# Kernel tuning notes

Hardware: AMD Instinct MI355X
Metric: run time of the kernel (lower is better)

Reference implementation:

```python
import jax, jax.numpy as jnp
import numpy as np
import math

B, S, E = 2, 2048, 1024
H, D = 16, 64
LAMBDA_INIT = 0.8
GN_EPS = 1e-5


def setup_inputs() -> dict:
    key = jax.random.key(0)
    ks = jax.random.split(key, 12)
    s = 0.02
    inputs = jax.random.normal(ks[0], (B, S, E), jnp.float32)
    attention_mask = jnp.ones((B, S), jnp.float32)
    token_indices = jnp.sort(jax.random.randint(ks[1], (B, S), 0, S), axis=-1)
    Wq = jax.random.normal(ks[2], (2 * H * D, E), jnp.float32) * s
    Wk = jax.random.normal(ks[3], (2 * H * D, E), jnp.float32) * s
    Wv = jax.random.normal(ks[4], (H * D, E), jnp.float32) * s
    Wo = jax.random.normal(ks[5], (E, H * D), jnp.float32) * s
    lam_q1 = jax.random.normal(ks[6], (D,), jnp.float32) * 0.1
    lam_q2 = jax.random.normal(ks[7], (D,), jnp.float32) * 0.1
    lam_k1 = jax.random.normal(ks[8], (D,), jnp.float32) * 0.1
    lam_k2 = jax.random.normal(ks[9], (D,), jnp.float32) * 0.1
    gn_w = jnp.ones((H * D,), jnp.float32)
    gn_b = jnp.zeros((H * D,), jnp.float32)
    return dict(inputs=inputs, attention_mask=attention_mask, token_indices=token_indices,
                Wq=Wq, Wk=Wk, Wv=Wv, Wo=Wo,
                lam_q1=lam_q1, lam_q2=lam_q2, lam_k1=lam_k1, lam_k2=lam_k2,
                gn_w=gn_w, gn_b=gn_b)


def reference(inputs, attention_mask, token_indices, Wq, Wk, Wv, Wo,
              lam_q1, lam_q2, lam_k1, lam_k2, gn_w, gn_b):
    b, s, e = inputs.shape
    # projections: q,k have doubled head dim (differential), v is standard
    q = (inputs @ Wq.T).reshape(b, s, H, 2 * D).transpose(0, 2, 1, 3)  # [B,H,S,2D]
    k = (inputs @ Wk.T).reshape(b, s, H, 2 * D).transpose(0, 2, 1, 3)
    v = (inputs @ Wv.T).reshape(b, s, H, D).transpose(0, 2, 1, 3)      # [B,H,S,D]
    Q1, Q2 = q[..., :D], q[..., D:]
    K1, K2 = k[..., :D], k[..., D:]
    scale = 1.0 / math.sqrt(D)
    s1 = jnp.einsum('bhqd,bhkd->bhqk', Q1, K1) * scale
    s2 = jnp.einsum('bhqd,bhkd->bhqk', Q2, K2) * scale
    # ALiBi bias: slopes[h] * (pos_q - pos_k), subtracted
    slopes = 2.0 ** (-8.0 * jnp.arange(1, H + 1, dtype=jnp.float32) / H)
    pos = token_indices.astype(jnp.float32)                            # [B,S]
    pos_diff = pos[:, :, None] - pos[:, None, :]                       # [B,S,S]
    bias = slopes[None, :, None, None] * pos_diff[:, None, :, :]       # [B,H,S,S]
    # causal + padding masks
    causal = jnp.triu(jnp.full((s, s), -1e9, jnp.float32), 1)[None, None]
    pad = (1.0 - attention_mask)[:, None, None, :] * -1e9
    s1 = s1 - bias + causal + pad
    s2 = s2 - bias + causal + pad
    w1 = jax.nn.softmax(s1, axis=-1)
    w2 = jax.nn.softmax(s2, axis=-1)
    lam = jnp.exp(jnp.dot(lam_q1, lam_k1)) - jnp.exp(jnp.dot(lam_q2, lam_k2)) + LAMBDA_INIT
    w = w1 - lam * w2
    out = jnp.einsum('bhqk,bhkd->bhqd', w, v)                          # [B,H,S,D]
    # GroupNorm(num_groups=H, num_channels=H*D) over channels-first layout [B,C,S]
    x = out.transpose(0, 2, 1, 3).reshape(b, s, H * D).transpose(0, 2, 1)  # [B,C,S]
    xg = x.reshape(b, H, D * s)
    mean = xg.mean(axis=-1, keepdims=True)
    var = xg.var(axis=-1, keepdims=True)
    xn = ((xg - mean) / jnp.sqrt(var + GN_EPS)).reshape(b, H * D, s)
    xn = xn * gn_w[None, :, None] + gn_b[None, :, None]
    xn = xn * (1.0 - LAMBDA_INIT)
    attn = xn.transpose(0, 2, 1)                                       # [B,S,H*D]
    return attn @ Wo.T
```

## Files before the change

kernel.cpp:

```cpp
#include <hip/hip_runtime.h>
#include <hip/hip_bf16.h>

typedef __hip_bfloat16 bf16;
typedef float f32x4 __attribute__((ext_vector_type(4)));
typedef float fvec4 __attribute__((ext_vector_type(4)));
typedef short s16x8 __attribute__((ext_vector_type(8)));

#define NB_B 2
#define NB_S 2048
#define NB_E 1024
#define NB_H 16
#define NB_D 64

typedef const __attribute__((address_space(1))) void* GPTR;
typedef __attribute__((address_space(3))) void* LPTR;

__device__ __forceinline__ void gld16(const void* g, void* l) {
  __builtin_amdgcn_global_load_lds((GPTR)g, (LPTR)l, 16, 0, 0);
}

__device__ __forceinline__ s16x8 ld8(const bf16* p) { return *(const s16x8*)p; }

__device__ __forceinline__ f32x4 MFMA(s16x8 a, s16x8 b, f32x4 c) {
  return __builtin_amdgcn_mfma_f32_16x16x32_bf16(a, b, c, 0, 0, 0);
}

struct __align__(8) bf16x4 { bf16 a, b, c, d; };

__global__ void prep_kernel(const float* __restrict__ inputs,
                            const float* __restrict__ wq, const float* __restrict__ wk,
                            const float* __restrict__ wv, const float* __restrict__ wo,
                            const float* __restrict__ lq1, const float* __restrict__ lq2,
                            const float* __restrict__ lk1, const float* __restrict__ lk2,
                            bf16* __restrict__ xbf,
                            bf16* __restrict__ oq, bf16* __restrict__ ok,
                            bf16* __restrict__ ov, bf16* __restrict__ oo,
                            float* __restrict__ lamo) {
  const int blk = blockIdx.x;
  if (blk < 4096) {
    int i = blk * 256 + threadIdx.x;
    fvec4 v = ((const fvec4*)inputs)[i];
    bf16x4 o = { bf16(v.x), bf16(v.y), bf16(v.z), bf16(v.w) };
    ((bf16x4*)xbf)[i] = o;
  } else if (blk < 10240) {
    int i = (blk - 4096) * 256 + threadIdx.x;
    const float* src; bf16* dst; int off;
    if (i < 524288)       { src = wq; dst = oq; off = i; }
    else if (i < 1048576) { src = wk; dst = ok; off = i - 524288; }
    else if (i < 1310720) { src = wv; dst = ov; off = i - 1048576; }
    else                  { src = wo; dst = oo; off = i - 1310720; }
    fvec4 v = ((const fvec4*)src)[off];
    bf16x4 o = { bf16(v.x), bf16(v.y), bf16(v.z), bf16(v.w) };
    ((bf16x4*)dst)[off] = o;
  } else {
    int l = threadIdx.x;
    if (l < 64) {
      float d1 = lq1[l] * lk1[l];
      float d2 = lq2[l] * lk2[l];
#pragma unroll
      for (int o = 32; o; o >>= 1) { d1 += __shfl_xor(d1, o); d2 += __shfl_xor(d2, o); }
      if (l == 0) lamo[0] = expf(d1) - expf(d2) + 0.8f;
    }
  }
}

__global__ void combo_kernel(const int* __restrict__ tok, const float* __restrict__ amask,
                             float* __restrict__ combo) {
  int i = blockIdx.x * 256 + threadIdx.x;
  int hh = i >> 12, bs = i & 4095;
  float slopeL = exp2f(-0.5f * (float)(hh + 1)) * 1.44269504088896340736f;
  combo[i] = slopeL * (float)tok[bs] + (amask[bs] - 1.f) * 1.44269504e9f;
}

template <int EPI>
__global__ __launch_bounds__(256) void gemm_bt(const bf16* __restrict__ A,
                                               const bf16* __restrict__ Bw,
                                               bf16* __restrict__ Ob,
                                               bf16* __restrict__ Ob2,
                                               bf16* __restrict__ Ob3,
                                               float* __restrict__ Of,
                                               int Kd, float oscale) {
  __shared__ bf16 As[2][128 * 32];
  __shared__ bf16 Bs[2][128 * 32];
  const int tid = threadIdx.x;
  const int lane = tid & 63;
  const int fr = lane & 15, fq = lane >> 4;
  const int wave = tid >> 6;
  const int wr = (wave >> 1) * 64, wc = (wave & 1) * 64;
  const size_t m0 = (size_t)blockIdx.x * 128, n0 = (size_t)blockIdx.y * 128;

  f32x4 acc[4][4];
#pragma unroll
  for (int i = 0; i < 4; i++)
#pragma unroll
    for (int j = 0; j < 4; j++) acc[i][j] = f32x4{0.f, 0.f, 0.f, 0.f};

  const int ca = tid, cb = tid + 256;
  const bf16* ga0 = A + (m0 + (ca >> 2)) * Kd + (ca & 3) * 8;
  const bf16* ga1 = A + (m0 + (cb >> 2)) * Kd + (cb & 3) * 8;
  const bf16* gb0 = Bw + (n0 + (ca >> 2)) * Kd + (ca & 3) * 8;
  const bf16* gb1 = Bw + (n0 + (cb >> 2)) * Kd + (cb & 3) * 8;

  gld16(ga0, &As[0][ca * 8]);
  gld16(ga1, &As[0][cb * 8]);
  gld16(gb0, &Bs[0][ca * 8]);
  gld16(gb1, &Bs[0][cb * 8]);
  __syncthreads();

  const int NKT = Kd >> 5;
  for (int kti = 0; kti < NKT; ++kti) {
    const int cur = kti & 1;
    if (kti + 1 < NKT) {
      const int kt = (kti + 1) << 5;
      gld16(ga0 + kt, &As[cur ^ 1][ca * 8]);
      gld16(ga1 + kt, &As[cur ^ 1][cb * 8]);
      gld16(gb0 + kt, &Bs[cur ^ 1][ca * 8]);
      gld16(gb1 + kt, &Bs[cur ^ 1][cb * 8]);
    }
    s16x8 af[4], bfv[4];
#pragma unroll
    for (int mi = 0; mi < 4; mi++) af[mi] = ld8(&As[cur][(wr + mi * 16 + fr) * 32 + fq * 8]);
#pragma unroll
    for (int ni = 0; ni < 4; ni++) bfv[ni] = ld8(&Bs[cur][(wc + ni * 16 + fr) * 32 + fq * 8]);
#pragma unroll
    for (int mi = 0; mi < 4; mi++)
#pragma unroll
      for (int ni = 0; ni < 4; ni++)
        acc[mi][ni] = MFMA(af[mi], bfv[ni], acc[mi][ni]);
    __syncthreads();
  }

  bf16* dst = Ob;
  size_t nsub = 0;
  float osc = oscale;
  bool isV = false;
  if constexpr (EPI == 0) {
    if (n0 >= 4096)      { dst = Ob3; nsub = 4096; osc = 1.0f; isV = true; }
    else if (n0 >= 2048) { dst = Ob2; nsub = 2048; osc = 1.0f; }
  }

  if constexpr (EPI == 0) {
    if (isV) {
#pragma unroll
      for (int mi = 0; mi < 4; mi++)
#pragma unroll
        for (int ni = 0; ni < 4; ni++) {
          size_t m = m0 + wr + mi * 16 + fq * 4;
          size_t n = n0 + wc + ni * 16 + fr;
          size_t nn = n - 4096;
          size_t b = m >> 11, s = m & 2047, h = nn >> 6, d = nn & 63;
          bf16x4 o = { bf16(acc[mi][ni][0]), bf16(acc[mi][ni][1]),
                       bf16(acc[mi][ni][2]), bf16(acc[mi][ni][3]) };
          *(bf16x4*)&dst[((b * NB_H + h) * NB_D + d) * NB_S + s] = o;
        }
    } else {
#pragma unroll
      for (int mi = 0; mi < 4; mi++)
#pragma unroll
        for (int ni = 0; ni < 4; ni++)
#pragma unroll
          for (int i = 0; i < 4; i++) {
            size_t m = m0 + wr + mi * 16 + fq * 4 + i;
            size_t n = n0 + wc + ni * 16 + fr;
            float v = acc[mi][ni][i] * osc;
            size_t nn = n - nsub;
            size_t b = m >> 11, s = m & 2047, h = nn >> 7, dd = nn & 127;
            dst[((b * NB_H + h) * NB_S + s) * 128 + dd] = bf16(v);
          }
    }
  } else {
#pragma unroll
    for (int mi = 0; mi < 4; mi++)
#pragma unroll
      for (int ni = 0; ni < 4; ni++)
#pragma unroll
        for (int i = 0; i < 4; i++) {
          size_t m = m0 + wr + mi * 16 + fq * 4 + i;
          size_t n = n0 + wc + ni * 16 + fr;
          Of[m * 1024 + n] = acc[mi][ni][i] * oscale;
        }
  }
}

__global__ __launch_bounds__(512, 2) void attn_kernel(
    const bf16* __restrict__ Q, const bf16* __restrict__ Kk, const bf16* __restrict__ Vt,
    const float* __restrict__ combo,
    const float* __restrict__ lamp, bf16* __restrict__ Xb, float* __restrict__ gnp) {
  __shared__ bf16 Ks[2][2][4096];
  __shared__ bf16 Vs[2][4096];
  __shared__ bf16 Ps[8][1024];
  __shared__ float gs[8][2];

  const int tid = threadIdx.x, lane = tid & 63, wave = tid >> 6;
  const int fr = lane & 15, fq = lane >> 4;
  const int id = blockIdx.x;
  const int w = id >> 3;
  const int bh = (id & 7) * 4 + (w & 3);
  const int qj = 15 - (w >> 2);
  const int b = bh >> 4, h = bh & 15;

  const float lam = lamp[0];
  const float* comboH = combo + ((size_t)h * NB_B + b) * NB_S;

  const bf16* Kbase = Kk + (size_t)bh * NB_S * 128;
  const bf16* Vbase = Vt + (size_t)bh * NB_D * NB_S;

  const s16x8 onesv = { 0x3F80, 0x3F80, 0x3F80, 0x3F80, 0x3F80, 0x3F80, 0x3F80, 0x3F80 };

  int adr[4][2], pw[4], pr[2];
#pragma unroll
  for (int nt = 0; nt < 4; nt++) {
    const int r = nt * 16 + fr;
#pragma unroll
    for (int kk = 0; kk < 2; kk++) adr[nt][kk] = r * 64 + (((kk * 4 + fq) ^ (r & 7)) << 3);
    pw[nt] = fr * 64 + (((nt * 4 + fq) ^ ((fr & 7) << 1)) << 2);
  }
  pr[0] = fr * 64 + (((fq * 2) ^ ((fr & 7) << 1)) << 2);
  pr[1] = fr * 64 + (((8 + fq * 2) ^ ((fr & 7) << 1)) << 2);

  const bf16* gK[2]; int lK[2];
#pragma unroll
  for (int i = 0; i < 2; i++) {
    int c = tid + i * 512, set = c >> 9, cc = c & 511;
    int row = cc >> 3, col8 = cc & 7, sc = col8 ^ (row & 7);
    gK[i] = Kbase + (size_t)row * 128 + set * 64 + sc * 8;
    lK[i] = set * 4096 + cc * 8;
  }
  const bf16* gV; int lV;
  {
    int c = tid;
    int row = c >> 3, col8 = c & 7, sc = col8 ^ (row & 7);
    gV = Vbase + (size_t)row * NB_S + sc * 8;
    lV = c * 8;
  }

  const int q0 = qj * 128;
  const int qw = q0 + wave * 16;
  const int ntiles = 2 * qj + 2;

  const bf16* qrow = Q + ((size_t)bh * NB_S + qw + fr) * 128;
  s16x8 q1[2], q2[2];
  q1[0] = ld8(qrow + fq * 8);       q1[1] = ld8(qrow + 32 + fq * 8);
  q2[0] = ld8(qrow + 64 + fq * 8);  q2[1] = ld8(qrow + 96 + fq * 8);

  const int qg = qw + fr;

  float m1 = -1e30f, m2 = -1e30f;
  f32x4 acc1[4], acc2[4];
  f32x4 accL1 = f32x4{0.f,0.f,0.f,0.f}, accL2 = f32x4{0.f,0.f,0.f,0.f};
#pragma unroll
  for (int nt = 0; nt < 4; nt++) { acc1[nt] = f32x4{0.f,0.f,0.f,0.f}; acc2[nt] = f32x4{0.f,0.f,0.f,0.f}; }

#pragma unroll
  for (int i = 0; i < 2; i++) gld16(gK[i], &Ks[0][0][0] + lK[i]);
  gld16(gV, &Vs[0][0] + lV);
  fvec4 cmb[4];
#pragma unroll
  for (int nt = 0; nt < 4; nt++) cmb[nt] = *(const fvec4*)(comboH + nt * 16 + fq * 4);
  __syncthreads();

  for (int t = 0; t < ntiles; ++t) {
    const int cur = t & 1;
    const int kv0 = t * 64;
    if (t + 1 < ntiles) {
#pragma unroll
      for (int i = 0; i < 2; i++)
        gld16(gK[i] + (size_t)(kv0 + 64) * 128, &Ks[cur ^ 1][0][0] + lK[i]);
      gld16(gV + (size_t)(kv0 + 64), &Vs[cur ^ 1][0] + lV);
    }

    const bool active = (kv0 <= qw + 15);
    if (active) {
      const bf16* kb0 = &Ks[cur][0][0];
      const bf16* kb1 = &Ks[cur][1][0];

      f32x4 c1[4], c2[4];
      __builtin_amdgcn_s_setprio(1);
#pragma unroll
      for (int nt = 0; nt < 4; nt++) {
        c1[nt] = MFMA(ld8(kb0 + adr[nt][0]), q1[0], cmb[nt]);
        c2[nt] = MFMA(ld8(kb1 + adr[nt][0]), q2[0], cmb[nt]);
      }
      {
        const float* cp = comboH + (t + 1 < ntiles ? kv0 + 64 : kv0);
#pragma unroll
        for (int nt = 0; nt < 4; nt++) cmb[nt] = *(const fvec4*)(cp + nt * 16 + fq * 4);
      }
#pragma unroll
      for (int nt = 0; nt < 4; nt++) {
        c1[nt] = MFMA(ld8(kb0 + adr[nt][1]), q1[1], c1[nt]);
        c2[nt] = MFMA(ld8(kb1 + adr[nt][1]), q2[1], c2[nt]);
      }
      __builtin_amdgcn_s_setprio(0);

      if (kv0 + 63 > qw) {
#pragma unroll
        for (int nt = 0; nt < 4; nt++)
#pragma unroll
          for (int i = 0; i < 4; i++)
            if (kv0 + nt * 16 + fq * 4 + i > qg) { c1[nt][i] = -1e30f; c2[nt][i] = -1e30f; }
      }

      s16x8 vf[4][2];
#pragma unroll
      for (int nt = 0; nt < 4; nt++)
#pragma unroll
        for (int kk = 0; kk < 2; kk++)
          vf[nt][kk] = ld8(&Vs[cur][adr[nt][kk]]);

      {
        float pm = fmaxf(fmaxf(fmaxf(c1[0][0], c1[0][1]), fmaxf(c1[0][2], c1[0][3])),
                         fmaxf(fmaxf(c1[1][0], c1[1][1]), fmaxf(c1[1][2], c1[1][3])));
        pm = fmaxf(pm, fmaxf(fmaxf(fmaxf(c1[2][0], c1[2][1]), fmaxf(c1[2][2], c1[2][3])),
                             fmaxf(fmaxf(c1[3][0], c1[3][1]), fmaxf(c1[3][2], c1[3][3]))));
        pm = fmaxf(pm, __shfl_xor(pm, 16));
        pm = fmaxf(pm, __shfl_xor(pm, 32));
        if (__any(pm > m1 + 8.f)) {
          const float nm = fmaxf(m1, pm);
          const float cor = exp2f(m1 - nm);
          m1 = nm;
#pragma unroll
          for (int i = 0; i < 4; i++) {
            const float ci = __shfl(cor, fq * 4 + i);
            accL1[i] *= ci;
#pragma unroll
            for (int nt = 0; nt < 4; nt++) acc1[nt][i] *= ci;
          }
        }
#pragma unroll
        for (int nt = 0; nt < 4; nt++) {
          bf16x4 pk = { bf16(exp2f(c1[nt][0] - m1)), bf16(exp2f(c1[nt][1] - m1)),
                        bf16(exp2f(c1[nt][2] - m1)), bf16(exp2f(c1[nt][3] - m1)) };
          *(bf16x4*)&Ps[wave][pw[nt]] = pk;
        }
        __builtin_amdgcn_s_setprio(1);
#pragma unroll
        for (int kk = 0; kk < 2; kk++) {
          const s16x8 pa = ld8(&Ps[wave][pr[kk]]);
          accL1 = MFMA(pa, onesv, accL1);
#pragma unroll
          for (int nt = 0; nt < 4; nt++) acc1[nt] = MFMA(pa, vf[nt][kk], acc1[nt]);
        }
        __builtin_amdgcn_s_setprio(0);
      }
      {
        float pm = fmaxf(fmaxf(fmaxf(c2[0][0], c2[0][1]), fmaxf(c2[0][2], c2[0][3])),
                         fmaxf(fmaxf(c2[1][0], c2[1][1]), fmaxf(c2[1][2], c2[1][3])));
        pm = fmaxf(pm, fmaxf(fmaxf(fmaxf(c2[2][0], c2[2][1]), fmaxf(c2[2][2], c2[2][3])),
                             fmaxf(fmaxf(c2[3][0], c2[3][1]), fmaxf(c2[3][2], c2[3][3]))));
        pm = fmaxf(pm, __shfl_xor(pm, 16));
        pm = fmaxf(pm, __shfl_xor(pm, 32));
        if (__any(pm > m2 + 8.f)) {
          const float nm = fmaxf(m2, pm);
          const float cor = exp2f(m2 - nm);
          m2 = nm;
#pragma unroll
          for (int i = 0; i < 4; i++) {
            const float ci = __shfl(cor, fq * 4 + i);
            accL2[i] *= ci;
#pragma unroll
            for (int nt = 0; nt < 4; nt++) acc2[nt][i] *= ci;
          }
        }
#pragma unroll
        for (int nt = 0; nt < 4; nt++) {
          bf16x4 pk = { bf16(exp2f(c2[nt][0] - m2)), bf16(exp2f(c2[nt][1] - m2)),
                        bf16(exp2f(c2[nt][2] - m2)), bf16(exp2f(c2[nt][3] - m2)) };
          *(bf16x4*)&Ps[wave][pw[nt]] = pk;
        }
        __builtin_amdgcn_s_setprio(1);
#pragma unroll
        for (int kk = 0; kk < 2; kk++) {
          const s16x8 pa = ld8(&Ps[wave][pr[kk]]);
          accL2 = MFMA(pa, onesv, accL2);
#pragma unroll
          for (int nt = 0; nt < 4; nt++) acc2[nt] = MFMA(pa, vf[nt][kk], acc2[nt]);
        }
        __builtin_amdgcn_s_setprio(0);
      }
    }

    __syncthreads();
  }

  float r1b[4], r2b[4];
#pragma unroll
  for (int i = 0; i < 4; i++) { r1b[i] = 1.f / accL1[i]; r2b[i] = lam / accL2[i]; }
  float s = 0.f, s2 = 0.f;
#pragma unroll
  for (int nt = 0; nt < 4; nt++)
#pragma unroll
    for (int i = 0; i < 4; i++) {
      const float v = acc1[nt][i] * r1b[i] - acc2[nt][i] * r2b[i];
      Xb[((size_t)bh * NB_S + qw + fq * 4 + i) * NB_D + nt * 16 + fr] = bf16(v);
      s += v; s2 += v * v;
    }
#pragma unroll
  for (int o = 32; o; o >>= 1) { s += __shfl_xor(s, o); s2 += __shfl_xor(s2, o); }
  if (lane == 0) { gs[wave][0] = s; gs[wave][1] = s2; }
  __syncthreads();
  if (tid == 0) {
    float S = 0.f, S2 = 0.f;
#pragma unroll
    for (int i = 0; i < 8; i++) { S += gs[i][0]; S2 += gs[i][1]; }
    atomicAdd(&gnp[bh * 2], S);
    atomicAdd(&gnp[bh * 2 + 1], S2);
  }
}

__global__ __launch_bounds__(256) void gn_apply(const bf16* __restrict__ Xb,
                                                const float* __restrict__ gnp,
                                                const float* __restrict__ gw,
                                                const float* __restrict__ gb,
                                                bf16* __restrict__ Xn) {
  const int blk = blockIdx.x, bh = blk >> 3, seg = blk & 7;
  const int b = bh >> 4, h = bh & 15;
  const float mean = gnp[bh * 2] * (1.f / 131072.f);
  const float var = gnp[bh * 2 + 1] * (1.f / 131072.f) - mean * mean;
  const float rstd = rsqrtf(var + 1e-5f) * 0.2f;
  const int tid = threadIdx.x;
  const int d0 = (tid * 8) & 63;
  const int c = h * 64 + d0;
  fvec4 w0 = *(const fvec4*)(gw + c), w1 = *(const fvec4*)(gw + c + 4);
  fvec4 b0 = *(const fvec4*)(gb + c), b1 = *(const fvec4*)(gb + c + 4);
  float wv[8] = { w0.x, w0.y, w0.z, w0.w, w1.x, w1.y, w1.z, w1.w };
  float bv[8] = { b0.x, b0.y, b0.z, b0.w, b1.x, b1.y, b1.z, b1.w };
  const bf16* xp = Xb + (size_t)bh * 131072;
#pragma unroll
  for (int jj = 0; jj < 8; jj++) {
    const int e = seg * 16384 + (tid + jj * 256) * 8;
    const int srow = e >> 6;
    s16x8 xv = *(const s16x8*)(xp + e);
    bf16 o8[8];
#pragma unroll
    for (int k = 0; k < 8; k++) {
      const float xf = __uint_as_float(((unsigned)(unsigned short)xv[k]) << 16);
      o8[k] = bf16((xf - mean) * rstd * wv[k] + 0.2f * bv[k]);
    }
    *(s16x8*)(Xn + ((size_t)b * NB_S + srow) * 1024 + c) = *(const s16x8*)o8;
  }
}

extern "C" void kernel_launch(void* const* d_in, const int* in_sizes, int n_in,
                              void* d_out, int out_size, void* d_ws, size_t ws_size,
                              hipStream_t stream) {
  const float* inputs = (const float*)d_in[0];
  const float* amask  = (const float*)d_in[1];
  const int*   tok    = (const int*)d_in[2];
  const float* Wq = (const float*)d_in[3];
  const float* Wk = (const float*)d_in[4];
  const float* Wv = (const float*)d_in[5];
  const float* Wo = (const float*)d_in[6];
  const float* lq1 = (const float*)d_in[7];
  const float* lq2 = (const float*)d_in[8];
  const float* lk1 = (const float*)d_in[9];
  const float* lk2 = (const float*)d_in[10];
  const float* gw = (const float*)d_in[11];
  const float* gb = (const float*)d_in[12];
  float* out = (float*)d_out;
  char* ws = (char*)d_ws;

  bf16* Xbf = (bf16*)(ws + 0);
  bf16* Wqb = (bf16*)(ws + 8388608);
  bf16* Wkb = (bf16*)(ws + 12582912);
  bf16* Wvb = (bf16*)(ws + 16777216);
  bf16* Xb  = (bf16*)(ws + 0);
  float* combo = (float*)(ws + 16777216);
  bf16* Qb  = (bf16*)(ws + 18874368);
  bf16* Xn  = (bf16*)(ws + 18874368);
  bf16* Kb  = (bf16*)(ws + 35651584);
  bf16* Vtb = (bf16*)(ws + 52428800);
  bf16* Wob = (bf16*)(ws + 60817408);
  float* lam = (float*)(ws + 62914560);
  float* gnp = (float*)(ws + 62914816);

  const float QSCALE = 0.125f * 1.44269504088896340736f;

  (void)hipMemsetAsync(gnp, 0, 512, stream);
  prep_kernel<<<10241, 256, 0, stream>>>(inputs, Wq, Wk, Wv, Wo, lq1, lq2, lk1, lk2,
                                         Xbf, Wqb, Wkb, Wvb, Wob, lam);

  gemm_bt<0><<<dim3(32, 40), 256, 0, stream>>>(Xbf, Wqb, Qb, Kb, Vtb, nullptr, 1024, QSCALE);

  combo_kernel<<<256, 256, 0, stream>>>(tok, amask, combo);

  attn_kernel<<<512, 512, 0, stream>>>(Qb, Kb, Vtb, combo, lam, Xb, gnp);

  gn_apply<<<256, 256, 0, stream>>>(Xb, gnp, gw, gb, Xn);

  gemm_bt<2><<<dim3(32, 8), 256, 0, stream>>>(Xn, Wob, nullptr, nullptr, nullptr, out, 1024, 1.0f);
}
```

Before: 200.9 us.

## Restructure attention into 4-wave blocks processing paired causal query tiles

The attention kernel goes from 8-wave blocks handling one 128-row query tile to 4-wave blocks that each process two 64-row query tiles (a long one and a short one, 31-pair and pair) in sequence. This balances the causal work per block and removes idle waves that previously skipped masked tiles. V is now single-buffered in LDS, staged through registers and written between two barriers per tile. Launch bounds change to 256 threads with 3 blocks per CU. The extra barriers per tile and the register-staged V path may add latency.

```diff
diff --git a/kernel.cpp b/kernel.cpp
--- a/kernel.cpp
+++ b/kernel.cpp
@@ -182,21 +182,21 @@
   }
 }
 
-__global__ __launch_bounds__(512, 2) void attn_kernel(
+__global__ __launch_bounds__(256, 3) void attn_kernel(
     const bf16* __restrict__ Q, const bf16* __restrict__ Kk, const bf16* __restrict__ Vt,
     const float* __restrict__ combo,
     const float* __restrict__ lamp, bf16* __restrict__ Xb, float* __restrict__ gnp) {
   __shared__ bf16 Ks[2][2][4096];
-  __shared__ bf16 Vs[2][4096];
-  __shared__ bf16 Ps[8][1024];
-  __shared__ float gs[8][2];
+  __shared__ bf16 Vs[4096];
+  __shared__ bf16 Ps[4][1024];
+  __shared__ float gs[4][2];
 
   const int tid = threadIdx.x, lane = tid & 63, wave = tid >> 6;
   const int fr = lane & 15, fq = lane >> 4;
   const int id = blockIdx.x;
-  const int w = id >> 3;
-  const int bh = (id & 7) * 4 + (w & 3);
-  const int qj = 15 - (w >> 2);
+  const int j = id >> 3;
+  const int bh = (id & 7) * 4 + (j & 3);
+  const int pair = j >> 2;
   const int b = bh >> 4, h = bh & 15;
 
   const float lam = lamp[0];
@@ -218,59 +218,64 @@
   pr[0] = fr * 64 + (((fq * 2) ^ ((fr & 7) << 1)) << 2);
   pr[1] = fr * 64 + (((8 + fq * 2) ^ ((fr & 7) << 1)) << 2);
 
-  const bf16* gK[2]; int lK[2];
-#pragma unroll
-  for (int i = 0; i < 2; i++) {
-    int c = tid + i * 512, set = c >> 9, cc = c & 511;
+  const bf16* gK[4]; int lK[4];
+#pragma unroll
+  for (int i = 0; i < 4; i++) {
+    int c = tid + i * 256, set = c >> 9, cc = c & 511;
     int row = cc >> 3, col8 = cc & 7, sc = col8 ^ (row & 7);
     gK[i] = Kbase + (size_t)row * 128 + set * 64 + sc * 8;
     lK[i] = set * 4096 + cc * 8;
   }
-  const bf16* gV; int lV;
-  {
-    int c = tid;
+  const bf16* gV[2]; int lV[2];
+#pragma unroll
+  for (int i = 0; i < 2; i++) {
+    int c = tid + i * 256;
     int row = c >> 3, col8 = c & 7, sc = col8 ^ (row & 7);
-    gV = Vbase + (size_t)row * NB_S + sc * 8;
-    lV = c * 8;
-  }
-
-  const int q0 = qj * 128;
-  const int qw = q0 + wave * 16;
-  const int ntiles = 2 * qj + 2;
-
-  const bf16* qrow = Q + ((size_t)bh * NB_S + qw + fr) * 128;
-  s16x8 q1[2], q2[2];
-  q1[0] = ld8(qrow + fq * 8);       q1[1] = ld8(qrow + 32 + fq * 8);
-  q2[0] = ld8(qrow + 64 + fq * 8);  q2[1] = ld8(qrow + 96 + fq * 8);
-
-  const int qg = qw + fr;
-
-  float m1 = -1e30f, m2 = -1e30f;
-  f32x4 acc1[4], acc2[4];
-  f32x4 accL1 = f32x4{0.f,0.f,0.f,0.f}, accL2 = f32x4{0.f,0.f,0.f,0.f};
-#pragma unroll
-  for (int nt = 0; nt < 4; nt++) { acc1[nt] = f32x4{0.f,0.f,0.f,0.f}; acc2[nt] = f32x4{0.f,0.f,0.f,0.f}; }
-
-#pragma unroll
-  for (int i = 0; i < 2; i++) gld16(gK[i], &Ks[0][0][0] + lK[i]);
-  gld16(gV, &Vs[0][0] + lV);
-  fvec4 cmb[4];
-#pragma unroll
-  for (int nt = 0; nt < 4; nt++) cmb[nt] = *(const fvec4*)(comboH + nt * 16 + fq * 4);
-  __syncthreads();
-
-  for (int t = 0; t < ntiles; ++t) {
-    const int cur = t & 1;
-    const int kv0 = t * 64;
-    if (t + 1 < ntiles) {
-#pragma unroll
-      for (int i = 0; i < 2; i++)
-        gld16(gK[i] + (size_t)(kv0 + 64) * 128, &Ks[cur ^ 1][0][0] + lK[i]);
-      gld16(gV + (size_t)(kv0 + 64), &Vs[cur ^ 1][0] + lV);
-    }
-
-    const bool active = (kv0 <= qw + 15);
-    if (active) {
+    gV[i] = Vbase + (size_t)row * NB_S + sc * 8;
+    lV[i] = c * 8;
+  }
+
+  float gss = 0.f, gq2 = 0.f;
+
+  for (int qpass = 0; qpass < 2; ++qpass) {
+    const int qb = qpass ? pair : (31 - pair);
+    const int q0 = qb * 64;
+    const int qw = q0 + wave * 16;
+    const int ntiles = qb + 1;
+    const int qg = qw + fr;
+
+    const bf16* qrow = Q + ((size_t)bh * NB_S + qw + fr) * 128;
+    s16x8 q1[2], q2[2];
+    q1[0] = ld8(qrow + fq * 8);       q1[1] = ld8(qrow + 32 + fq * 8);
+    q2[0] = ld8(qrow + 64 + fq * 8);  q2[1] = ld8(qrow + 96 + fq * 8);
+
+    float m1 = -1e30f, m2 = -1e30f;
+    f32x4 acc1[4], acc2[4];
+    f32x4 accL1 = f32x4{0.f,0.f,0.f,0.f}, accL2 = f32x4{0.f,0.f,0.f,0.f};
+#pragma unroll
+    for (int nt = 0; nt < 4; nt++) { acc1[nt] = f32x4{0.f,0.f,0.f,0.f}; acc2[nt] = f32x4{0.f,0.f,0.f,0.f}; }
+
+#pragma unroll
+    for (int i = 0; i < 4; i++) gld16(gK[i], &Ks[0][0][0] + lK[i]);
+#pragma unroll
+    for (int i = 0; i < 2; i++) gld16(gV[i], &Vs[0] + lV[i]);
+    fvec4 cmb[4];
+#pragma unroll
+    for (int nt = 0; nt < 4; nt++) cmb[nt] = *(const fvec4*)(comboH + nt * 16 + fq * 4);
+    __syncthreads();
+
+    for (int t = 0; t < ntiles; ++t) {
+      const int cur = t & 1;
+      const int kv0 = t * 64;
+      fvec4 vreg[2];
+      if (t + 1 < ntiles) {
+#pragma unroll
+        for (int i = 0; i < 2; i++) vreg[i] = *(const fvec4*)(gV[i] + (size_t)(kv0 + 64));
+#pragma unroll
+        for (int i = 0; i < 4; i++)
+          gld16(gK[i] + (size_t)(kv0 + 64) * 128, &Ks[cur ^ 1][0][0] + lK[i]);
+      }
+
       const bf16* kb0 = &Ks[cur][0][0];
       const bf16* kb1 = &Ks[cur][1][0];
 
@@ -293,7 +298,7 @@
       }
       __builtin_amdgcn_s_setprio(0);
 
-      if (kv0 + 63 > qw) {
+      if (t == ntiles - 1) {
 #pragma unroll
         for (int nt = 0; nt < 4; nt++)
 #pragma unroll
@@ -306,7 +311,7 @@
       for (int nt = 0; nt < 4; nt++)
 #pragma unroll
         for (int kk = 0; kk < 2; kk++)
-          vf[nt][kk] = ld8(&Vs[cur][adr[nt][kk]]);
+          vf[nt][kk] = ld8(&Vs[adr[nt][kk]]);
 
       {
         float pm = fmaxf(fmaxf(fmaxf(c1[0][0], c1[0][1]), fmaxf(c1[0][2], c1[0][3])),
@@ -378,31 +383,36 @@
         }
         __builtin_amdgcn_s_setprio(0);
       }
+
+      __syncthreads();
+      if (t + 1 < ntiles) {
+#pragma unroll
+        for (int i = 0; i < 2; i++) *(fvec4*)(&Vs[lV[i]]) = vreg[i];
+      }
+      __syncthreads();
     }
 
-    __syncthreads();
-  }
-
-  float r1b[4], r2b[4];
-#pragma unroll
-  for (int i = 0; i < 4; i++) { r1b[i] = 1.f / accL1[i]; r2b[i] = lam / accL2[i]; }
-  float s = 0.f, s2 = 0.f;
-#pragma unroll
-  for (int nt = 0; nt < 4; nt++)
-#pragma unroll
-    for (int i = 0; i < 4; i++) {
-      const float v = acc1[nt][i] * r1b[i] - acc2[nt][i] * r2b[i];
-      Xb[((size_t)bh * NB_S + qw + fq * 4 + i) * NB_D + nt * 16 + fr] = bf16(v);
-      s += v; s2 += v * v;
-    }
-#pragma unroll
-  for (int o = 32; o; o >>= 1) { s += __shfl_xor(s, o); s2 += __shfl_xor(s2, o); }
-  if (lane == 0) { gs[wave][0] = s; gs[wave][1] = s2; }
+    float r1b[4], r2b[4];
+#pragma unroll
+    for (int i = 0; i < 4; i++) { r1b[i] = 1.f / accL1[i]; r2b[i] = lam / accL2[i]; }
+#pragma unroll
+    for (int nt = 0; nt < 4; nt++)
+#pragma unroll
+      for (int i = 0; i < 4; i++) {
+        const float v = acc1[nt][i] * r1b[i] - acc2[nt][i] * r2b[i];
+        Xb[((size_t)bh * NB_S + qw + fq * 4 + i) * NB_D + nt * 16 + fr] = bf16(v);
+        gss += v; gq2 += v * v;
+      }
+  }
+
+#pragma unroll
+  for (int o = 32; o; o >>= 1) { gss += __shfl_xor(gss, o); gq2 += __shfl_xor(gq2, o); }
+  if (lane == 0) { gs[wave][0] = gss; gs[wave][1] = gq2; }
   __syncthreads();
   if (tid == 0) {
     float S = 0.f, S2 = 0.f;
 #pragma unroll
-    for (int i = 0; i < 8; i++) { S += gs[i][0]; S2 += gs[i][1]; }
+    for (int i = 0; i < 4; i++) { S += gs[i][0]; S2 += gs[i][1]; }
     atomicAdd(&gnp[bh * 2], S);
     atomicAdd(&gnp[bh * 2 + 1], S2);
   }
@@ -484,7 +494,7 @@
 
   combo_kernel<<<256, 256, 0, stream>>>(tok, amask, combo);
 
-  attn_kernel<<<512, 512, 0, stream>>>(Qb, Kb, Vtb, combo, lam, Xb, gnp);
+  attn_kernel<<<512, 256, 0, stream>>>(Qb, Kb, Vtb, combo, lam, Xb, gnp);
 
   gn_apply<<<256, 256, 0, stream>>>(Xb, gnp, gw, gb, Xn);
 
```

After: 278.4 us. +38.6%, slower.

## Fuse GroupNorm apply into output projection GEMM A-tile loads

Applied to the files above, without the earlier changes.

Removes the standalone gn_apply pass and its Xn intermediate. A small gn_coef kernel folds mean, rstd, weight and bias into per-(batch,channel) scale and shift vectors. The output GEMM then reads the head-major attention output directly and applies the scale and shift while staging A tiles into shared memory. This saves one write and one read of the activation tensor, but the A loads now go through registers instead of async global-to-LDS copies, and each A tile is normalized once per N-block, so the normalization work is repeated across the 8 N-blocks.

```diff
diff --git a/kernel.cpp b/kernel.cpp
--- a/kernel.cpp
+++ b/kernel.cpp
@@ -72,6 +72,20 @@
   combo[i] = slopeL * (float)tok[bs] + (amask[bs] - 1.f) * 1.44269504e9f;
 }
 
+__global__ void gn_coef(const float* __restrict__ gnp, const float* __restrict__ gw,
+                        const float* __restrict__ gb,
+                        float* __restrict__ Sc, float* __restrict__ Tc) {
+  int i = blockIdx.x * 256 + threadIdx.x;
+  int b = i >> 10, c = i & 1023;
+  int bh = b * 16 + (c >> 6);
+  float mean = gnp[bh * 2] * (1.f / 131072.f);
+  float var = gnp[bh * 2 + 1] * (1.f / 131072.f) - mean * mean;
+  float rstd = rsqrtf(var + 1e-5f) * 0.2f;
+  float S = rstd * gw[c];
+  Sc[i] = S;
+  Tc[i] = 0.2f * gb[c] - mean * S;
+}
+
 template <int EPI>
 __global__ __launch_bounds__(256) void gemm_bt(const bf16* __restrict__ A,
                                                const bf16* __restrict__ Bw,
@@ -182,6 +196,104 @@
   }
 }
 
+__device__ __forceinline__ s16x8 gn_chunk(const bf16* __restrict__ Xb, size_t base, int tb,
+                                          int k, const float* __restrict__ Sc,
+                                          const float* __restrict__ Tc) {
+  s16x8 xv = *(const s16x8*)(Xb + base + (size_t)(k >> 6) * 131072 + (k & 63));
+  const float* sp = Sc + tb + k;
+  const float* tp = Tc + tb + k;
+  fvec4 s0v = *(const fvec4*)sp, s1v = *(const fvec4*)(sp + 4);
+  fvec4 t0v = *(const fvec4*)tp, t1v = *(const fvec4*)(tp + 4);
+  float sv[8] = { s0v.x, s0v.y, s0v.z, s0v.w, s1v.x, s1v.y, s1v.z, s1v.w };
+  float tv[8] = { t0v.x, t0v.y, t0v.z, t0v.w, t1v.x, t1v.y, t1v.z, t1v.w };
+  bf16 o8[8];
+#pragma unroll
+  for (int j = 0; j < 8; j++) {
+    const float xf = __uint_as_float(((unsigned)(unsigned short)xv[j]) << 16);
+    o8[j] = bf16(xf * sv[j] + tv[j]);
+  }
+  return *(const s16x8*)o8;
+}
+
+__global__ __launch_bounds__(256) void gemm_out(const bf16* __restrict__ Xb,
+                                                const bf16* __restrict__ Bw,
+                                                const float* __restrict__ Sc,
+                                                const float* __restrict__ Tc,
+                                                float* __restrict__ Of) {
+  __shared__ bf16 As[2][128 * 32];
+  __shared__ bf16 Bs[2][128 * 32];
+  const int tid = threadIdx.x;
+  const int lane = tid & 63;
+  const int fr = lane & 15, fq = lane >> 4;
+  const int wave = tid >> 6;
+  const int wr = (wave >> 1) * 64, wc = (wave & 1) * 64;
+  const size_t m0 = (size_t)blockIdx.x * 128, n0 = (size_t)blockIdx.y * 128;
+
+  f32x4 acc[4][4];
+#pragma unroll
+  for (int i = 0; i < 4; i++)
+#pragma unroll
+    for (int j = 0; j < 4; j++) acc[i][j] = f32x4{0.f, 0.f, 0.f, 0.f};
+
+  const int ca = tid, cb = tid + 256;
+  const int ma = (int)m0 + (ca >> 2), mb = (int)m0 + (cb >> 2);
+  const int koa = (ca & 3) * 8, kob = (cb & 3) * 8;
+  const size_t basea = (size_t)(ma >> 11) * 2097152 + (size_t)(ma & 2047) * 64;
+  const size_t baseb = (size_t)(mb >> 11) * 2097152 + (size_t)(mb & 2047) * 64;
+  const int tba = (ma >> 11) * 1024, tbb = (mb >> 11) * 1024;
+
+  const bf16* gb0 = Bw + (n0 + (ca >> 2)) * 1024 + koa;
+  const bf16* gb1 = Bw + (n0 + (cb >> 2)) * 1024 + kob;
+
+  {
+    s16x8 a0 = gn_chunk(Xb, basea, tba, koa, Sc, Tc);
+    s16x8 a1 = gn_chunk(Xb, baseb, tbb, kob, Sc, Tc);
+    gld16(gb0, &Bs[0][ca * 8]);
+    gld16(gb1, &Bs[0][cb * 8]);
+    *(s16x8*)&As[0][ca * 8] = a0;
+    *(s16x8*)&As[0][cb * 8] = a1;
+  }
+  __syncthreads();
+
+  for (int kti = 0; kti < 32; ++kti) {
+    const int cur = kti & 1;
+    s16x8 na0, na1;
+    if (kti + 1 < 32) {
+      const int kt = (kti + 1) << 5;
+      na0 = gn_chunk(Xb, basea, tba, kt + koa, Sc, Tc);
+      na1 = gn_chunk(Xb, baseb, tbb, kt + kob, Sc, Tc);
+      gld16(gb0 + kt, &Bs[cur ^ 1][ca * 8]);
+      gld16(gb1 + kt, &Bs[cur ^ 1][cb * 8]);
+    }
+    s16x8 af[4], bfv[4];
+#pragma unroll
+    for (int mi = 0; mi < 4; mi++) af[mi] = ld8(&As[cur][(wr + mi * 16 + fr) * 32 + fq * 8]);
+#pragma unroll
+    for (int ni = 0; ni < 4; ni++) bfv[ni] = ld8(&Bs[cur][(wc + ni * 16 + fr) * 32 + fq * 8]);
+#pragma unroll
+    for (int mi = 0; mi < 4; mi++)
+#pragma unroll
+      for (int ni = 0; ni < 4; ni++)
+        acc[mi][ni] = MFMA(af[mi], bfv[ni], acc[mi][ni]);
+    if (kti + 1 < 32) {
+      *(s16x8*)&As[cur ^ 1][ca * 8] = na0;
+      *(s16x8*)&As[cur ^ 1][cb * 8] = na1;
+    }
+    __syncthreads();
+  }
+
+#pragma unroll
+  for (int mi = 0; mi < 4; mi++)
+#pragma unroll
+    for (int ni = 0; ni < 4; ni++)
+#pragma unroll
+      for (int i = 0; i < 4; i++) {
+        size_t m = m0 + wr + mi * 16 + fq * 4 + i;
+        size_t n = n0 + wc + ni * 16 + fr;
+        Of[m * 1024 + n] = acc[mi][ni][i];
+      }
+}
+
 __global__ __launch_bounds__(512, 2) void attn_kernel(
     const bf16* __restrict__ Q, const bf16* __restrict__ Kk, const bf16* __restrict__ Vt,
     const float* __restrict__ combo,
@@ -405,39 +517,6 @@
     for (int i = 0; i < 8; i++) { S += gs[i][0]; S2 += gs[i][1]; }
     atomicAdd(&gnp[bh * 2], S);
     atomicAdd(&gnp[bh * 2 + 1], S2);
-  }
-}
-
-__global__ __launch_bounds__(256) void gn_apply(const bf16* __restrict__ Xb,
-                                                const float* __restrict__ gnp,
-                                                const float* __restrict__ gw,
-                                                const float* __restrict__ gb,
-                                                bf16* __restrict__ Xn) {
-  const int blk = blockIdx.x, bh = blk >> 3, seg = blk & 7;
-  const int b = bh >> 4, h = bh & 15;
-  const float mean = gnp[bh * 2] * (1.f / 131072.f);
-  const float var = gnp[bh * 2 + 1] * (1.f / 131072.f) - mean * mean;
-  const float rstd = rsqrtf(var + 1e-5f) * 0.2f;
-  const int tid = threadIdx.x;
-  const int d0 = (tid * 8) & 63;
-  const int c = h * 64 + d0;
-  fvec4 w0 = *(const fvec4*)(gw + c), w1 = *(const fvec4*)(gw + c + 4);
-  fvec4 b0 = *(const fvec4*)(gb + c), b1 = *(const fvec4*)(gb + c + 4);
-  float wv[8] = { w0.x, w0.y, w0.z, w0.w, w1.x, w1.y, w1.z, w1.w };
-  float bv[8] = { b0.x, b0.y, b0.z, b0.w, b1.x, b1.y, b1.z, b1.w };
-  const bf16* xp = Xb + (size_t)bh * 131072;
-#pragma unroll
-  for (int jj = 0; jj < 8; jj++) {
-    const int e = seg * 16384 + (tid + jj * 256) * 8;
-    const int srow = e >> 6;
-    s16x8 xv = *(const s16x8*)(xp + e);
-    bf16 o8[8];
-#pragma unroll
-    for (int k = 0; k < 8; k++) {
-      const float xf = __uint_as_float(((unsigned)(unsigned short)xv[k]) << 16);
-      o8[k] = bf16((xf - mean) * rstd * wv[k] + 0.2f * bv[k]);
-    }
-    *(s16x8*)(Xn + ((size_t)b * NB_S + srow) * 1024 + c) = *(const s16x8*)o8;
   }
 }
 
@@ -467,12 +546,13 @@
   bf16* Xb  = (bf16*)(ws + 0);
   float* combo = (float*)(ws + 16777216);
   bf16* Qb  = (bf16*)(ws + 18874368);
-  bf16* Xn  = (bf16*)(ws + 18874368);
   bf16* Kb  = (bf16*)(ws + 35651584);
   bf16* Vtb = (bf16*)(ws + 52428800);
   bf16* Wob = (bf16*)(ws + 60817408);
   float* lam = (float*)(ws + 62914560);
   float* gnp = (float*)(ws + 62914816);
+  float* Sc  = (float*)(ws + 62915584);
+  float* Tc  = (float*)(ws + 62923776);
 
   const float QSCALE = 0.125f * 1.44269504088896340736f;
 
@@ -486,7 +566,7 @@
 
   attn_kernel<<<512, 512, 0, stream>>>(Qb, Kb, Vtb, combo, lam, Xb, gnp);
 
-  gn_apply<<<256, 256, 0, stream>>>(Xb, gnp, gw, gb, Xn);
-
-  gemm_bt<2><<<dim3(32, 8), 256, 0, stream>>>(Xn, Wob, nullptr, nullptr, nullptr, out, 1024, 1.0f);
-}
+  gn_coef<<<8, 256, 0, stream>>>(gnp, gw, gb, Sc, Tc);
+
+  gemm_out<<<dim3(32, 8), 256, 0, stream>>>(Xb, Wob, Sc, Tc, out);
+}
```

New measurement: 212.3 us. +5.7%, slower.
